# Kernel tuning notes

Hardware: AMD Instinct MI355X
Metric: run time of the kernel (lower is better)

## Reference

```python
import jax, jax.numpy as jnp
import numpy as np


def _sobel_kernels():
    sx = np.array([[[-1, 0, 1], [-2, 0, 2], [-1, 0, 1]],
                   [[-2, 0, 2], [-4, 0, 4], [-2, 0, 2]],
                   [[-1, 0, 1], [-2, 0, 2], [-1, 0, 1]]], dtype=np.float32)
    sy = np.array([[[-1, -2, -1], [0, 0, 0], [1, 2, 1]],
                   [[-2, -4, -2], [0, 0, 0], [2, 4, 2]],
                   [[-1, -2, -1], [0, 0, 0], [1, 2, 1]]], dtype=np.float32)
    sz = np.array([[[1, 2, 1], [2, 4, 2], [1, 2, 1]],
                   [[0, 0, 0], [0, 0, 0], [0, 0, 0]],
                   [[-1, -2, -1], [-2, -4, -2], [-1, -2, -1]]], dtype=np.float32)
    # Stack as a single 3-output-channel conv: [O=3, I=1, 3, 3, 3]
    return jnp.asarray(np.stack([sx, sy, sz])[:, None])


def _conv3d(x, k):
    # x: [B, 1, D, H, W], k: [3, 1, 3, 3, 3] -> [B, 3, D, H, W]
    return jax.lax.conv_general_dilated(
        x, k, window_strides=(1, 1, 1), padding=[(1, 1)] * 3,
        dimension_numbers=('NCDHW', 'OIDHW', 'NCDHW'))


def setup_inputs() -> dict:
    key = jax.random.key(0)
    k1, k2 = jax.random.split(key)
    shape = (2, 1, 160, 192, 160)
    moved = jax.random.normal(k1, shape, dtype=jnp.float32)
    label = jax.random.normal(k2, shape, dtype=jnp.float32)
    return {"moved": moved, "label": label}


def reference(moved, label):
    k = _sobel_kernels()
    gm = _conv3d(moved, k)   # [B, 3, D, H, W]: x/y/z gradients
    gl = _conv3d(label, k)
    # per-direction L1 means (mean over B,D,H,W for each of the 3 channels)
    per_dir = jnp.mean(jnp.abs(gm - gl), axis=(0, 2, 3, 4))
    # original takes abs of each (already nonneg) loss, then averages
    return jnp.mean(jnp.abs(per_dir))
```

## Files before the change

kernel.cpp:

```cpp
#include <hip/hip_runtime.h>
#include <stdint.h>


#define BB 2
#define DD 160
#define HH 192
#define WW 160
#define HW (HH * WW)
#define NTOT (BB * DD * HW)

#define TH 8
#define DC 10
#define NIT (DC + 2)
#define PROWS (TH + 2)
#define PFLOATS (PROWS * WW)
#define PPAD 1792
#define NTHREADS 256
#define WPT 5

#define AS1 __attribute__((address_space(1)))
#define AS3 __attribute__((address_space(3)))

__device__ __forceinline__ void dma16(const float* g, float* l) {
    __builtin_amdgcn_global_load_lds((const AS1 void*)g, (AS3 void*)l, 16, 0, 0);
}

__global__ __launch_bounds__(NTHREADS) void sobel_loss_kernel(
    const float* __restrict__ moved, const float* __restrict__ label,
    float* __restrict__ out)
{
    __shared__ float sm[3][PPAD];
    __shared__ float sl[3][PPAD];
    __shared__ float red[NTHREADS / 64];

    const int tid = threadIdx.x;
    const int h0  = blockIdx.x * TH;
    const int d0  = blockIdx.y * DC;
    const int b   = blockIdx.z;
    const int base_b = b * (DD * HW);

    const bool do2 = (tid < 192);

    const int hl    = tid >> 5;
    const int wbase = (tid & 31) * WPT;

    const bool rv0 = (h0 + hl) > 0;
    const bool rv2 = (h0 + hl + 1) < HH;

    auto stage = [&](int pl, int s) {
        if ((unsigned)pl >= (unsigned)DD) return;
        const int pstart = base_b + pl * HW + (h0 - 1) * WW;
        int g0 = pstart + tid * 4;
        g0 = min(max(g0, 0), NTOT - 4);
        dma16(moved + g0, &sm[s][tid * 4]);
        dma16(label + g0, &sl[s][tid * 4]);
        if (do2) {
            int g1 = pstart + (tid + NTHREADS) * 4;
            g1 = min(max(g1, 0), NTOT - 4);
            dma16(moved + g1, &sm[s][(tid + NTHREADS) * 4]);
            dma16(label + g1, &sl[s][(tid + NTHREADS) * 4]);
        }
    };

    float pxm1[WPT], pxm2[WPT], pym1[WPT], pym2[WPT], pzm1[WPT], pzm2[WPT];
#pragma unroll
    for (int k = 0; k < WPT; ++k) {
        pxm1[k] = pxm2[k] = 0.f;
        pym1[k] = pym2[k] = 0.f;
        pzm1[k] = pzm2[k] = 0.f;
    }
    float acc = 0.f;

    stage(d0 - 1, 0);
    stage(d0,     1);
    __syncthreads();

    for (int it = 0; it < NIT; ++it) {
        if (it + 2 < NIT) stage(d0 - 1 + (it + 2), (it + 2) % 3);

        const int s = it % 3;
        const float* mb = sm[s];
        const float* lb = sl[s];
        const bool pv = (unsigned)(d0 - 1 + it) < (unsigned)DD;

        const bool v0 = pv && rv0;
        const bool v1 = pv;
        const bool v2 = pv && rv2;
        const int o0 = hl * WW;
        const int o1 = o0 + WW;
        const int o2 = o1 + WW;

        float cS[WPT + 2], cD[WPT + 2];
#pragma unroll
        for (int x = 0; x < WPT + 2; ++x) {
            const int w  = wbase - 1 + x;
            const bool wv = (unsigned)w < (unsigned)WW;
            const int wc = wv ? w : (w < 0 ? 0 : WW - 1);
            const float a  = (v0 && wv) ? (mb[o0 + wc] - lb[o0 + wc]) : 0.f;
            const float m  = (v1 && wv) ? (mb[o1 + wc] - lb[o1 + wc]) : 0.f;
            const float c2 = (v2 && wv) ? (mb[o2 + wc] - lb[o2 + wc]) : 0.f;
            cS[x] = (a + c2) + 2.f * m;
            cD[x] = c2 - a;
        }
#pragma unroll
        for (int k = 0; k < WPT; ++k) {
            const float px = cS[k + 2] - cS[k];
            const float pz = (cS[k] + cS[k + 2]) + 2.f * cS[k + 1];
            const float py = (cD[k] + cD[k + 2]) + 2.f * cD[k + 1];
            if (it >= 2) {
                const float gx = pxm2[k] + 2.f * pxm1[k] + px;
                const float gy = pym2[k] + 2.f * pym1[k] + py;
                const float gz = pzm2[k] - pz;
                acc += fabsf(gx) + fabsf(gy) + fabsf(gz);
            }
            pxm2[k] = pxm1[k]; pxm1[k] = px;
            pym2[k] = pym1[k]; pym1[k] = py;
            pzm2[k] = pzm1[k]; pzm1[k] = pz;
        }

        __syncthreads();
    }

#pragma unroll
    for (int off = 32; off > 0; off >>= 1)
        acc += __shfl_down(acc, off, 64);
    if ((tid & 63) == 0) red[tid >> 6] = acc;
    __syncthreads();
    if (tid == 0) {
        const float s = red[0] + red[1] + red[2] + red[3];
        atomicAdd(out, s * (1.0f / (3.0f * BB * DD * HH * WW)));
    }
}

extern "C" void kernel_launch(void* const* d_in, const int* in_sizes, int n_in,
                              void* d_out, int out_size, void* d_ws, size_t ws_size,
                              hipStream_t stream) {
    const float* moved = (const float*)d_in[0];
    const float* label = (const float*)d_in[1];
    float* out = (float*)d_out;
    (void)in_sizes; (void)n_in; (void)out_size; (void)d_ws; (void)ws_size;

    hipMemsetAsync(out, 0, sizeof(float), stream);
    dim3 grid(HH / TH, DD / DC, BB);
    sobel_loss_kernel<<<grid, NTHREADS, 0, stream>>>(moved, label, out);
}
```

Baseline: 120.3 us.

## Halve depth chunk, double-buffer LDS planes, and raise occupancy with launch bounds

Halves the depth chunk per block, which doubles the grid, and switches from a triple-buffered to a double-buffered LDS plane ring. Each step now prefetches only one plane ahead. LDS use per block drops, and `__launch_bounds__(NTHREADS, 6)` asks for more resident blocks. Halo rows outside the volume are skipped rather than loaded through clamped addresses. The aim is more parallelism and latency hiding, at the cost of a larger depth-halo reload fraction (7 planes per 5 instead of 12 per 10) and a shallower prefetch distance.

Result: slower. 334.1 us (+177.8%).

```diff
diff --git a/kernel.cpp b/kernel.cpp
--- a/kernel.cpp
+++ b/kernel.cpp
@@ -7,14 +7,13 @@
 #define HH 192
 #define WW 160
 #define HW (HH * WW)
-#define NTOT (BB * DD * HW)
 
 #define TH 8
-#define DC 10
+#define DC 5
 #define NIT (DC + 2)
 #define PROWS (TH + 2)
 #define PFLOATS (PROWS * WW)
-#define PPAD 1792
+#define NQUADS (PFLOATS / 4)
 #define NTHREADS 256
 #define WPT 5
 
@@ -25,12 +24,12 @@
     __builtin_amdgcn_global_load_lds((const AS1 void*)g, (AS3 void*)l, 16, 0, 0);
 }
 
-__global__ __launch_bounds__(NTHREADS) void sobel_loss_kernel(
+__global__ __launch_bounds__(NTHREADS, 6) void sobel_loss_kernel(
     const float* __restrict__ moved, const float* __restrict__ label,
     float* __restrict__ out)
 {
-    __shared__ float sm[3][PPAD];
-    __shared__ float sl[3][PPAD];
+    __shared__ float sm[2][PFLOATS];
+    __shared__ float sl[2][PFLOATS];
     __shared__ float red[NTHREADS / 64];
 
     const int tid = threadIdx.x;
@@ -39,28 +38,25 @@
     const int b   = blockIdx.z;
     const int base_b = b * (DD * HW);
 
-    const bool do2 = (tid < 192);
-
-    const int hl    = tid >> 5;
-    const int wbase = (tid & 31) * WPT;
-
-    const bool rv0 = (h0 + hl) > 0;
-    const bool rv2 = (h0 + hl + 1) < HH;
+    const int q1 = tid + NTHREADS;
+    const int gr0 = h0 - 1 + tid / 40;
+    const int gr1 = h0 - 1 + q1 / 40;
+    const bool hv0 = (unsigned)gr0 < (unsigned)HH;
+    const bool hv1 = (q1 < NQUADS) && ((unsigned)gr1 < (unsigned)HH);
 
     auto stage = [&](int pl, int s) {
         if ((unsigned)pl >= (unsigned)DD) return;
         const int pstart = base_b + pl * HW + (h0 - 1) * WW;
-        int g0 = pstart + tid * 4;
-        g0 = min(max(g0, 0), NTOT - 4);
-        dma16(moved + g0, &sm[s][tid * 4]);
-        dma16(label + g0, &sl[s][tid * 4]);
-        if (do2) {
-            int g1 = pstart + (tid + NTHREADS) * 4;
-            g1 = min(max(g1, 0), NTOT - 4);
-            dma16(moved + g1, &sm[s][(tid + NTHREADS) * 4]);
-            dma16(label + g1, &sl[s][(tid + NTHREADS) * 4]);
-        }
+        if (hv0) { dma16(moved + pstart + tid * 4, &sm[s][tid * 4]);
+                   dma16(label + pstart + tid * 4, &sl[s][tid * 4]); }
+        if (hv1) { dma16(moved + pstart + q1 * 4, &sm[s][q1 * 4]);
+                   dma16(label + pstart + q1 * 4, &sl[s][q1 * 4]); }
     };
+
+    const int hl    = tid >> 5;
+    const int wbase = (tid & 31) * WPT;
+    const bool rv0 = (h0 + hl) > 0;
+    const bool rv2 = (h0 + hl + 1) < HH;
 
     float pxm1[WPT], pxm2[WPT], pym1[WPT], pym2[WPT], pzm1[WPT], pzm2[WPT];
 #pragma unroll
@@ -72,19 +68,17 @@
     float acc = 0.f;
 
     stage(d0 - 1, 0);
-    stage(d0,     1);
     __syncthreads();
 
     for (int it = 0; it < NIT; ++it) {
-        if (it + 2 < NIT) stage(d0 - 1 + (it + 2), (it + 2) % 3);
+        if (it + 1 < NIT) stage(d0 + it, (it + 1) & 1);
 
-        const int s = it % 3;
+        const int s = it & 1;
         const float* mb = sm[s];
         const float* lb = sl[s];
         const bool pv = (unsigned)(d0 - 1 + it) < (unsigned)DD;
 
         const bool v0 = pv && rv0;
-        const bool v1 = pv;
         const bool v2 = pv && rv2;
         const int o0 = hl * WW;
         const int o1 = o0 + WW;
@@ -97,7 +91,7 @@
             const bool wv = (unsigned)w < (unsigned)WW;
             const int wc = wv ? w : (w < 0 ? 0 : WW - 1);
             const float a  = (v0 && wv) ? (mb[o0 + wc] - lb[o0 + wc]) : 0.f;
-            const float m  = (v1 && wv) ? (mb[o1 + wc] - lb[o1 + wc]) : 0.f;
+            const float m  = (pv && wv) ? (mb[o1 + wc] - lb[o1 + wc]) : 0.f;
             const float c2 = (v2 && wv) ? (mb[o2 + wc] - lb[o2 + wc]) : 0.f;
             cS[x] = (a + c2) + 2.f * m;
             cD[x] = c2 - a;
```
